# Optimization experiments

Measured on AMD Instinct MI355X. Metric: run time of the kernel, lower is better.

## Reference

```python
import jax, jax.numpy as jnp
import numpy as np
from functools import partial

HID = 16
EMB = 32

def setup_inputs() -> dict:
    key = jax.random.key(0)
    ks = jax.random.split(key, 9)
    S, B, V = 64, 32, 50257
    stdv = 1.0 / np.sqrt(HID)
    u = lambda k, shp: jax.random.uniform(k, shp, jnp.float32, -stdv, stdv)
    return {
        "input_batch": jax.random.randint(ks[0], (S, B), 0, V),
        "embedding": u(ks[1], (V, EMB)),  # original re-inits randn embedding with uniform via init_params
        "W_lr": u(ks[2], (HID, EMB + HID)),
        "b_lr": u(ks[3], (HID,)),
        "W_rl": u(ks[4], (HID, EMB + HID)),
        "b_rl": u(ks[5], (HID,)),
        "W_ho": u(ks[6], (V, 2 * HID)),
        "b_ho": u(ks[7], (V,)),
        "h0": u(ks[8], (1, HID)),
    }


def _rnn_pre_states(emb, W, b, h0):
    # emb: [S,B,E]; returns stacked hidden states BEFORE each step: [S,B,H]
    def step(h, x):
        h_new = jnp.tanh(jnp.concatenate([x, h], axis=-1) @ W.T + b)
        return h_new, h  # collect pre-update state
    _, pre = jax.lax.scan(step, h0, emb)
    return pre


def reference(input_batch, embedding, W_lr, b_lr, W_rl, b_rl, W_ho, b_ho, h0):
    S, B = input_batch.shape
    emb = embedding[input_batch]                      # [S,B,EMB]
    h0b = jnp.broadcast_to(h0, (B, HID))
    # Left-to-right: prediction at i uses hLR state before consuming word i
    hLR_pre = _rnn_pre_states(emb, W_lr, b_lr, h0b)   # [S,B,HID]
    # Right-to-left: run over reversed sequence, collect pre-states, reverse back
    hRL_pre = _rnn_pre_states(emb[::-1], W_rl, b_rl, h0b)[::-1]  # [S,B,HID]
    h = jnp.concatenate([hLR_pre, hRL_pre], axis=-1)  # [S,B,2*HID]
    logits = jnp.einsum('sbh,vh->sbv', h, W_ho) + b_ho
    return jax.nn.log_softmax(logits, axis=-1)        # [S,B,V]
```

## Files before the change

kernel.cpp:

```cpp
#include <hip/hip_runtime.h>
#include <hip/hip_bf16.h>

#define S 64
#define B 32
#define HID 16
#define EMB 32
#define V 50257
#define NT 3142
#define VP (NT*16)
#define NCHUNK 16
#define TPC 197
#define M 2048
#define PREP_BLOCKS 6284

using bf16x8 = __attribute__((ext_vector_type(8))) __bf16;
using f32x4  = __attribute__((ext_vector_type(4))) float;

__global__ void k_prep(const float* __restrict__ W_ho, const float* __restrict__ b_ho,
                       const int* __restrict__ idx, const float* __restrict__ emb,
                       const float* __restrict__ W_lr, const float* __restrict__ b_lr,
                       const float* __restrict__ W_rl, const float* __restrict__ b_rl,
                       __bf16* __restrict__ Wb, float* __restrict__ bias,
                       float* __restrict__ P) {
    const int bx = blockIdx.x;
    if (bx < PREP_BLOCKS) {
        int i = bx * 256 + threadIdx.x;
        if (i < VP) bias[i] = (i < V) ? b_ho[i] : -1e30f;
        int v = i >> 5;
        Wb[i] = (v < V) ? (__bf16)W_ho[i] : (__bf16)0.f;
    } else {
        int i = (bx - PREP_BLOCKS) * 256 + threadIdx.x;
        const int dir = i >> 15, r = i & 32767, m = r >> 4, j = r & 15;
        const float* W  = dir ? W_rl : W_lr;
        const float* bb = dir ? b_rl : b_lr;
        const int tok = idx[m];
        const float4* er = reinterpret_cast<const float4*>(emb + (size_t)tok * EMB);
        const float4* wr = reinterpret_cast<const float4*>(W + j * (EMB + HID));
        float acc = bb[j];
        #pragma unroll
        for (int q = 0; q < 8; ++q) {
            float4 e4 = er[q], w4 = wr[q];
            acc += e4.x * w4.x + e4.y * w4.y + e4.z * w4.z + e4.w * w4.w;
        }
        P[i] = acc;
    }
}

__global__ void k_rnn(const float* __restrict__ P,
                      const float* __restrict__ W_lr, const float* __restrict__ W_rl,
                      const float* __restrict__ h0, __bf16* __restrict__ hcat) {
    __shared__ float Psh[S * 4 * HID];
    __shared__ float hsh[4][17];
    const int t = threadIdx.x;
    const int dir = blockIdx.x >> 3, bq = blockIdx.x & 7;
    const int bl = t >> 4, j = t & 15;
    const int b = bq * 4 + bl;
    {
        const float4* Pg4 = reinterpret_cast<const float4*>(P);
        float4* Ps4 = reinterpret_cast<float4*>(Psh);
        #pragma unroll
        for (int i = 0; i < 16; ++i) {
            int s = (t >> 4) + 4 * i;
            Ps4[t + 64 * i] = Pg4[dir * 8192 + s * 128 + bq * 16 + (t & 15)];
        }
    }
    const float* Wd = (dir ? W_rl : W_lr) + j * (EMB + HID) + EMB;
    float wh[16];
    #pragma unroll
    for (int q = 0; q < 4; ++q) {
        float4 w4 = *reinterpret_cast<const float4*>(Wd + q * 4);
        wh[q * 4 + 0] = w4.x; wh[q * 4 + 1] = w4.y;
        wh[q * 4 + 2] = w4.z; wh[q * 4 + 3] = w4.w;
    }
    float hcur = h0[j];
    hsh[bl][j] = hcur;
    __syncthreads();
    for (int step = 0; step < S; ++step) {
        const int s = dir ? (S - 1 - step) : step;
        hcat[(s * B + b) * 32 + dir * HID + j] = (__bf16)hcur;
        float acc = Psh[s * 64 + bl * 16 + j];
        #pragma unroll
        for (int k = 0; k < HID; ++k) acc += wh[k] * hsh[bl][k];
        hcur = tanhf(acc);
        __syncthreads();
        hsh[bl][j] = hcur;
        __syncthreads();
    }
}

__global__ void k_pass1(const __bf16* __restrict__ hb, const __bf16* __restrict__ Wb,
                        const float* __restrict__ bias, float* __restrict__ partials) {
    const int chunk = blockIdx.x, rt = blockIdx.y;
    const int wave = threadIdx.x >> 6, lane = threadIdx.x & 63;
    const int lr = lane & 15, kg = lane >> 4;
    const int m0 = rt * 16;
    const bf16x8 a = *reinterpret_cast<const bf16x8*>(hb + (m0 + lr) * 32 + kg * 8);
    const f32x4 zero = {0.f, 0.f, 0.f, 0.f};
    float s0 = 0.f, s1 = 0.f, s2 = 0.f, s3 = 0.f;
    const int t0 = chunk * TPC;
    const int t1 = (t0 + TPC < NT) ? (t0 + TPC) : NT;
    for (int tt = t0 + wave; tt < t1; tt += 4) {
        const int v0 = tt * 16;
        bf16x8 bf = *reinterpret_cast<const bf16x8*>(Wb + (v0 + lr) * 32 + kg * 8);
        float bc = bias[v0 + lr];
        f32x4 d = __builtin_amdgcn_mfma_f32_16x16x32_bf16(a, bf, zero, 0, 0, 0);
        s0 += __expf(d[0] + bc);
        s1 += __expf(d[1] + bc);
        s2 += __expf(d[2] + bc);
        s3 += __expf(d[3] + bc);
    }
    #pragma unroll
    for (int off = 1; off < 16; off <<= 1) {
        s0 += __shfl_xor(s0, off);
        s1 += __shfl_xor(s1, off);
        s2 += __shfl_xor(s2, off);
        s3 += __shfl_xor(s3, off);
    }
    __shared__ float red[4][16];
    if (lr == 0) {
        red[wave][kg * 4 + 0] = s0;
        red[wave][kg * 4 + 1] = s1;
        red[wave][kg * 4 + 2] = s2;
        red[wave][kg * 4 + 3] = s3;
    }
    __syncthreads();
    if (threadIdx.x < 16) {
        float tot = red[0][threadIdx.x] + red[1][threadIdx.x] +
                    red[2][threadIdx.x] + red[3][threadIdx.x];
        partials[(m0 + threadIdx.x) * NCHUNK + chunk] = tot;
    }
}

__global__ void k_pass2(const __bf16* __restrict__ hb, const __bf16* __restrict__ Wb,
                        const float* __restrict__ bias, const float* __restrict__ partials,
                        float* __restrict__ out) {
    __shared__ float stage[16][260];
    __shared__ float logZsh[16];
    const int t = threadIdx.x;
    const int wave = t >> 6, lane = t & 63;
    const int lr = lane & 15, kg = lane >> 4;
    const int m0 = blockIdx.y * 16;
    const int cb = blockIdx.x * 256;
    if (t < 16) {
        float tot = 0.f;
        #pragma unroll
        for (int c = 0; c < NCHUNK; ++c) tot += partials[(m0 + t) * NCHUNK + c];
        logZsh[t] = logf(tot);
    }
    const bf16x8 a = *reinterpret_cast<const bf16x8*>(hb + (m0 + lr) * 32 + kg * 8);
    const f32x4 zero = {0.f, 0.f, 0.f, 0.f};
    #pragma unroll
    for (int q = 0; q < 4; ++q) {
        const int tt = blockIdx.x * 16 + wave * 4 + q;
        if (tt < NT) {
            const int v0 = tt * 16;
            bf16x8 bf = *reinterpret_cast<const bf16x8*>(Wb + (v0 + lr) * 32 + kg * 8);
            float bc = bias[v0 + lr];
            f32x4 d = __builtin_amdgcn_mfma_f32_16x16x32_bf16(a, bf, zero, 0, 0, 0);
            const int cl = wave * 64 + q * 16 + lr;
            #pragma unroll
            for (int r = 0; r < 4; ++r)
                stage[kg * 4 + r][cl] = d[r] + bc;
        }
    }
    __syncthreads();
    #pragma unroll
    for (int r = 0; r < 4; ++r) {
        const int row = wave * 4 + r;
        const float lz = logZsh[row];
        const size_t R = (size_t)(m0 + row) * V;
        #pragma unroll
        for (int it = 0; it < 4; ++it) {
            const int c = it * 64 + lane;
            const int col = cb + c;
            if (col < V) out[R + col] = stage[row][c] - lz;
        }
    }
}

extern "C" void kernel_launch(void* const* d_in, const int* in_sizes, int n_in,
                              void* d_out, int out_size, void* d_ws, size_t ws_size,
                              hipStream_t stream) {
    const int*   idx       = (const int*)d_in[0];
    const float* embedding = (const float*)d_in[1];
    const float* W_lr      = (const float*)d_in[2];
    const float* b_lr      = (const float*)d_in[3];
    const float* W_rl      = (const float*)d_in[4];
    const float* b_rl      = (const float*)d_in[5];
    const float* W_ho      = (const float*)d_in[6];
    const float* b_ho      = (const float*)d_in[7];
    const float* h0        = (const float*)d_in[8];
    float* out = (float*)d_out;

    char* ws = (char*)d_ws;
    size_t off = 0;
    __bf16* Wb      = (__bf16*)(ws + off); off += (size_t)VP * EMB * 2;
    float*  bias    = (float*)(ws + off);  off += (size_t)VP * 4;
    __bf16* hb      = (__bf16*)(ws + off); off += (size_t)M * 32 * 2;
    float*  P       = (float*)(ws + off);  off += (size_t)2 * M * HID * 4;
    float*  partials= (float*)(ws + off);  off += (size_t)M * NCHUNK * 4;

    k_prep<<<PREP_BLOCKS + 256, 256, 0, stream>>>(W_ho, b_ho, idx, embedding,
                                                  W_lr, b_lr, W_rl, b_rl, Wb, bias, P);
    k_rnn<<<16, 64, 0, stream>>>(P, W_lr, W_rl, h0, hb);
    k_pass1<<<dim3(NCHUNK, M / 16), 256, 0, stream>>>(hb, Wb, bias, partials);
    k_pass2<<<dim3(197, M / 16), 256, 0, stream>>>(hb, Wb, bias, partials, out);
}
```

Baseline: 198.7 us.

## Keep vocab weight fragments in registers and loop over row tiles

```diff
diff --git a/kernel.cpp b/kernel.cpp
--- a/kernel.cpp
+++ b/kernel.cpp
@@ -6,12 +6,12 @@
 #define HID 16
 #define EMB 32
 #define V 50257
-#define NT 3142
-#define VP (NT*16)
-#define NCHUNK 16
-#define TPC 197
+#define NCB 197
+#define VP2 (NCB*256)
 #define M 2048
-#define PREP_BLOCKS 6284
+#define PREP_BLOCKS (VP2*EMB/256)
+#define NRG 4
+#define RT_PER (128/NRG)
 
 using bf16x8 = __attribute__((ext_vector_type(8))) __bf16;
 using f32x4  = __attribute__((ext_vector_type(4))) float;
@@ -25,7 +25,7 @@
     const int bx = blockIdx.x;
     if (bx < PREP_BLOCKS) {
         int i = bx * 256 + threadIdx.x;
-        if (i < VP) bias[i] = (i < V) ? b_ho[i] : -1e30f;
+        if (i < VP2) bias[i] = (i < V) ? b_ho[i] : -1e30f;
         int v = i >> 5;
         Wb[i] = (v < V) ? (__bf16)W_ho[i] : (__bf16)0.f;
     } else {
@@ -74,7 +74,6 @@
     }
     float hcur = h0[j];
     hsh[bl][j] = hcur;
-    __syncthreads();
     for (int step = 0; step < S; ++step) {
         const int s = dir ? (S - 1 - step) : step;
         hcat[(s * B + b) * 32 + dir * HID + j] = (__bf16)hcur;
@@ -82,99 +81,110 @@
         #pragma unroll
         for (int k = 0; k < HID; ++k) acc += wh[k] * hsh[bl][k];
         hcur = tanhf(acc);
-        __syncthreads();
         hsh[bl][j] = hcur;
-        __syncthreads();
     }
 }
 
 __global__ void k_pass1(const __bf16* __restrict__ hb, const __bf16* __restrict__ Wb,
                         const float* __restrict__ bias, float* __restrict__ partials) {
-    const int chunk = blockIdx.x, rt = blockIdx.y;
+    const int cbx = blockIdx.x, rg = blockIdx.y;
     const int wave = threadIdx.x >> 6, lane = threadIdx.x & 63;
     const int lr = lane & 15, kg = lane >> 4;
-    const int m0 = rt * 16;
-    const bf16x8 a = *reinterpret_cast<const bf16x8*>(hb + (m0 + lr) * 32 + kg * 8);
+    const int ttbase = cbx * 16 + wave * 4;
+    bf16x8 wfrag[4]; float bc[4];
+    #pragma unroll
+    for (int q = 0; q < 4; ++q) {
+        wfrag[q] = *reinterpret_cast<const bf16x8*>(Wb + ((ttbase + q) * 16 + lr) * 32 + kg * 8);
+        bc[q] = bias[(ttbase + q) * 16 + lr];
+    }
+    __shared__ float red[4][16];
     const f32x4 zero = {0.f, 0.f, 0.f, 0.f};
-    float s0 = 0.f, s1 = 0.f, s2 = 0.f, s3 = 0.f;
-    const int t0 = chunk * TPC;
-    const int t1 = (t0 + TPC < NT) ? (t0 + TPC) : NT;
-    for (int tt = t0 + wave; tt < t1; tt += 4) {
-        const int v0 = tt * 16;
-        bf16x8 bf = *reinterpret_cast<const bf16x8*>(Wb + (v0 + lr) * 32 + kg * 8);
-        float bc = bias[v0 + lr];
-        f32x4 d = __builtin_amdgcn_mfma_f32_16x16x32_bf16(a, bf, zero, 0, 0, 0);
-        s0 += __expf(d[0] + bc);
-        s1 += __expf(d[1] + bc);
-        s2 += __expf(d[2] + bc);
-        s3 += __expf(d[3] + bc);
-    }
-    #pragma unroll
-    for (int off = 1; off < 16; off <<= 1) {
-        s0 += __shfl_xor(s0, off);
-        s1 += __shfl_xor(s1, off);
-        s2 += __shfl_xor(s2, off);
-        s3 += __shfl_xor(s3, off);
-    }
-    __shared__ float red[4][16];
-    if (lr == 0) {
-        red[wave][kg * 4 + 0] = s0;
-        red[wave][kg * 4 + 1] = s1;
-        red[wave][kg * 4 + 2] = s2;
-        red[wave][kg * 4 + 3] = s3;
-    }
-    __syncthreads();
-    if (threadIdx.x < 16) {
-        float tot = red[0][threadIdx.x] + red[1][threadIdx.x] +
-                    red[2][threadIdx.x] + red[3][threadIdx.x];
-        partials[(m0 + threadIdx.x) * NCHUNK + chunk] = tot;
-    }
+    for (int rt = rg * RT_PER; rt < rg * RT_PER + RT_PER; ++rt) {
+        const int m0 = rt * 16;
+        const bf16x8 a = *reinterpret_cast<const bf16x8*>(hb + (m0 + lr) * 32 + kg * 8);
+        float s0 = 0.f, s1 = 0.f, s2 = 0.f, s3 = 0.f;
+        #pragma unroll
+        for (int q = 0; q < 4; ++q) {
+            f32x4 d = __builtin_amdgcn_mfma_f32_16x16x32_bf16(a, wfrag[q], zero, 0, 0, 0);
+            s0 += __expf(d[0] + bc[q]);
+            s1 += __expf(d[1] + bc[q]);
+            s2 += __expf(d[2] + bc[q]);
+            s3 += __expf(d[3] + bc[q]);
+        }
+        #pragma unroll
+        for (int off = 1; off < 16; off <<= 1) {
+            s0 += __shfl_xor(s0, off);
+            s1 += __shfl_xor(s1, off);
+            s2 += __shfl_xor(s2, off);
+            s3 += __shfl_xor(s3, off);
+        }
+        if (lr == 0) {
+            red[wave][kg * 4 + 0] = s0;
+            red[wave][kg * 4 + 1] = s1;
+            red[wave][kg * 4 + 2] = s2;
+            red[wave][kg * 4 + 3] = s3;
+        }
+        __syncthreads();
+        if (threadIdx.x < 16)
+            partials[cbx * M + m0 + threadIdx.x] =
+                red[0][threadIdx.x] + red[1][threadIdx.x] +
+                red[2][threadIdx.x] + red[3][threadIdx.x];
+        __syncthreads();
+    }
+}
+
+__global__ void k_reduce(const float* __restrict__ partials, float* __restrict__ logZ) {
+    int r = blockIdx.x * 256 + threadIdx.x;
+    float tot = 0.f;
+    for (int c = 0; c < NCB; ++c) tot += partials[c * M + r];
+    logZ[r] = logf(tot);
 }
 
 __global__ void k_pass2(const __bf16* __restrict__ hb, const __bf16* __restrict__ Wb,
-                        const float* __restrict__ bias, const float* __restrict__ partials,
+                        const float* __restrict__ bias, const float* __restrict__ logZ,
                         float* __restrict__ out) {
     __shared__ float stage[16][260];
-    __shared__ float logZsh[16];
-    const int t = threadIdx.x;
-    const int wave = t >> 6, lane = t & 63;
+    const int cbx = blockIdx.x, rg = blockIdx.y;
+    const int wave = threadIdx.x >> 6, lane = threadIdx.x & 63;
     const int lr = lane & 15, kg = lane >> 4;
-    const int m0 = blockIdx.y * 16;
-    const int cb = blockIdx.x * 256;
-    if (t < 16) {
-        float tot = 0.f;
-        #pragma unroll
-        for (int c = 0; c < NCHUNK; ++c) tot += partials[(m0 + t) * NCHUNK + c];
-        logZsh[t] = logf(tot);
-    }
-    const bf16x8 a = *reinterpret_cast<const bf16x8*>(hb + (m0 + lr) * 32 + kg * 8);
-    const f32x4 zero = {0.f, 0.f, 0.f, 0.f};
+    const int ttbase = cbx * 16 + wave * 4;
+    bf16x8 wfrag[4]; float bc[4];
     #pragma unroll
     for (int q = 0; q < 4; ++q) {
-        const int tt = blockIdx.x * 16 + wave * 4 + q;
-        if (tt < NT) {
-            const int v0 = tt * 16;
-            bf16x8 bf = *reinterpret_cast<const bf16x8*>(Wb + (v0 + lr) * 32 + kg * 8);
-            float bc = bias[v0 + lr];
-            f32x4 d = __builtin_amdgcn_mfma_f32_16x16x32_bf16(a, bf, zero, 0, 0, 0);
+        wfrag[q] = *reinterpret_cast<const bf16x8*>(Wb + ((ttbase + q) * 16 + lr) * 32 + kg * 8);
+        bc[q] = bias[(ttbase + q) * 16 + lr];
+    }
+    const int cb = cbx * 256;
+    const f32x4 zero = {0.f, 0.f, 0.f, 0.f};
+    for (int rt = rg * RT_PER; rt < rg * RT_PER + RT_PER; ++rt) {
+        const int m0 = rt * 16;
+        const bf16x8 a = *reinterpret_cast<const bf16x8*>(hb + (m0 + lr) * 32 + kg * 8);
+        #pragma unroll
+        for (int q = 0; q < 4; ++q) {
+            f32x4 d = __builtin_amdgcn_mfma_f32_16x16x32_bf16(a, wfrag[q], zero, 0, 0, 0);
             const int cl = wave * 64 + q * 16 + lr;
             #pragma unroll
             for (int r = 0; r < 4; ++r)
-                stage[kg * 4 + r][cl] = d[r] + bc;
-        }
-    }
-    __syncthreads();
-    #pragma unroll
-    for (int r = 0; r < 4; ++r) {
-        const int row = wave * 4 + r;
-        const float lz = logZsh[row];
-        const size_t R = (size_t)(m0 + row) * V;
-        #pragma unroll
-        for (int it = 0; it < 4; ++it) {
-            const int c = it * 64 + lane;
-            const int col = cb + c;
-            if (col < V) out[R + col] = stage[row][c] - lz;
-        }
+                stage[kg * 4 + r][cl] = d[r] + bc[q];
+        }
+        asm volatile("s_waitcnt lgkmcnt(0)" ::: "memory");
+        __builtin_amdgcn_s_barrier();
+        __builtin_amdgcn_sched_barrier(0);
+        #pragma unroll
+        for (int r = 0; r < 4; ++r) {
+            const int row = wave * 4 + r;
+            const float lz = logZ[m0 + row];
+            const size_t R = (size_t)(m0 + row) * V;
+            #pragma unroll
+            for (int it = 0; it < 4; ++it) {
+                const int c = it * 64 + lane;
+                const int col = cb + c;
+                if (col < V) out[R + col] = stage[row][c] - lz;
+            }
+        }
+        asm volatile("s_waitcnt lgkmcnt(0)" ::: "memory");
+        __builtin_amdgcn_s_barrier();
+        __builtin_amdgcn_sched_barrier(0);
     }
 }
 
@@ -194,15 +204,17 @@
 
     char* ws = (char*)d_ws;
     size_t off = 0;
-    __bf16* Wb      = (__bf16*)(ws + off); off += (size_t)VP * EMB * 2;
-    float*  bias    = (float*)(ws + off);  off += (size_t)VP * 4;
+    __bf16* Wb      = (__bf16*)(ws + off); off += (size_t)VP2 * EMB * 2;
+    float*  bias    = (float*)(ws + off);  off += (size_t)VP2 * 4;
     __bf16* hb      = (__bf16*)(ws + off); off += (size_t)M * 32 * 2;
     float*  P       = (float*)(ws + off);  off += (size_t)2 * M * HID * 4;
-    float*  partials= (float*)(ws + off);  off += (size_t)M * NCHUNK * 4;
+    float*  partials= (float*)(ws + off);  off += (size_t)NCB * M * 4;
+    float*  logZ    = (float*)(ws + off);  off += (size_t)M * 4;
 
     k_prep<<<PREP_BLOCKS + 256, 256, 0, stream>>>(W_ho, b_ho, idx, embedding,
                                                   W_lr, b_lr, W_rl, b_rl, Wb, bias, P);
     k_rnn<<<16, 64, 0, stream>>>(P, W_lr, W_rl, h0, hb);
-    k_pass1<<<dim3(NCHUNK, M / 16), 256, 0, stream>>>(hb, Wb, bias, partials);
-    k_pass2<<<dim3(197, M / 16), 256, 0, stream>>>(hb, Wb, bias, partials, out);
-}
+    k_pass1<<<dim3(NCB, NRG), 256, 0, stream>>>(hb, Wb, bias, partials);
+    k_reduce<<<8, 256, 0, stream>>>(partials, logZ);
+    k_pass2<<<dim3(NCB, NRG), 256, 0, stream>>>(hb, Wb, bias, logZ, out);
+}
```

New measurement: 200.0 us. About the same (+0.7%).
